# Performance work log

Hardware: AMD Instinct MI355X
Metric: run time of the kernel (lower is better)

The kernel has to match this reference:

```python
import jax, jax.numpy as jnp
import numpy as np

HEADS = 2
OUT_CH = 128
NEG_SLOPE_ATT = 0.2   # GATv2Conv attention LeakyReLU
NEG_SLOPE_ACT = 0.01  # nn.LeakyReLU default
BN_EPS = 1e-5


def setup_inputs() -> dict:
    key = jax.random.key(0)
    ks = jax.random.split(key, 8)
    B, C, D, H, W = 2, 128, 8, 32, 32
    N = B * D * H * W            # 16384 graph nodes
    E = 196608                   # avg degree 12
    x = jax.random.normal(ks[0], (B, C, D, H, W), dtype=jnp.float32)
    edge_index = jax.random.randint(ks[1], (2, E), 0, N, dtype=jnp.int64)
    lin_w = jax.random.normal(ks[2], (C, HEADS * OUT_CH), dtype=jnp.float32) * (1.0 / np.sqrt(C))
    lin_b = jax.random.normal(ks[3], (HEADS * OUT_CH,), dtype=jnp.float32) * 0.02
    att = jax.random.normal(ks[4], (HEADS, OUT_CH), dtype=jnp.float32) * (1.0 / np.sqrt(OUT_CH))
    gat_bias = jax.random.normal(ks[5], (OUT_CH,), dtype=jnp.float32) * 0.02
    bn_gamma = jnp.ones((OUT_CH,), dtype=jnp.float32)
    bn_beta = jnp.zeros((OUT_CH,), dtype=jnp.float32)
    return {"x": x, "edge_index": edge_index, "lin_w": lin_w, "lin_b": lin_b,
            "att": att, "gat_bias": gat_bias, "bn_gamma": bn_gamma, "bn_beta": bn_beta}


def _gatv2(xf, src, dst, lin_w, lin_b, att, gat_bias, n_nodes):
    # shared-weights GATv2: x' = x W + b, per edge e=(j->i): score = a . lrelu(x'_i + x'_j)
    h = (xf @ lin_w + lin_b).reshape(n_nodes, HEADS, OUT_CH)  # [N, H, C]
    x_src = h[src]                                            # [E, H, C] messages
    logits = jnp.einsum('ehc,hc->eh', jax.nn.leaky_relu(x_src + h[dst], NEG_SLOPE_ATT), att)
    # segment softmax over edges sharing the same target node
    m = jax.ops.segment_max(logits, dst, num_segments=n_nodes)      # [N, H]
    ex = jnp.exp(logits - m[dst])
    denom = jax.ops.segment_sum(ex, dst, num_segments=n_nodes)      # [N, H]
    alpha = ex / denom[dst]
    out = jax.ops.segment_sum(x_src * alpha[..., None], dst, num_segments=n_nodes)  # [N, H, C]
    return out.mean(axis=1) + gat_bias  # concat=False -> head mean


def reference(x, edge_index, lin_w, lin_b, att, gat_bias, bn_gamma, bn_beta):
    B, C, D, H, W = x.shape
    N = B * D * H * W
    xf = x.reshape(B, C, -1).transpose(0, 2, 1).reshape(N, C)
    # add_self_loops=True (PyG default)
    loop = jnp.arange(N, dtype=edge_index.dtype)
    src = jnp.concatenate([edge_index[0], loop])
    dst = jnp.concatenate([edge_index[1], loop])
    out = _gatv2(xf, src, dst, lin_w, lin_b, att, gat_bias, N)      # [N, OUT_CH]
    out = out.reshape(B, D * H * W, OUT_CH).transpose(0, 2, 1).reshape(B, OUT_CH, D, H, W)
    # BatchNorm3d (training-mode batch stats, biased variance)
    mean = out.mean(axis=(0, 2, 3, 4), keepdims=True)
    var = out.var(axis=(0, 2, 3, 4), keepdims=True)
    out = (out - mean) / jnp.sqrt(var + BN_EPS)
    out = out * bn_gamma.reshape(1, -1, 1, 1, 1) + bn_beta.reshape(1, -1, 1, 1, 1)
    return jax.nn.leaky_relu(out, NEG_SLOPE_ACT)
```

## Files before the change

kernel.cpp:

```cpp
#include <hip/hip_runtime.h>
#include <math.h>

#define N_NODES 16384
#define CIN 128
#define HOUT 256
#define OUTC 128
#define NEG_ATT 0.2f
#define NEG_ACT 0.01f
#define BN_EPS 1e-5f

typedef short short8 __attribute__((ext_vector_type(8)));
typedef float f32x4 __attribute__((ext_vector_type(4)));

static __device__ __forceinline__ unsigned short f2bf(float f) {
    unsigned int u = __float_as_uint(f);
    unsigned int r = (u + 0x7FFFu + ((u >> 16) & 1u)) >> 16;
    return (unsigned short)r;
}
static __device__ __forceinline__ float bf2f(unsigned short s) {
    return __uint_as_float(((unsigned int)s) << 16);
}
static __device__ __forceinline__ void loadbf8(const unsigned short* p, float* f) {
    uint4 u = *(const uint4*)p;
    f[0] = __uint_as_float(u.x << 16);
    f[1] = __uint_as_float(u.x & 0xffff0000u);
    f[2] = __uint_as_float(u.y << 16);
    f[3] = __uint_as_float(u.y & 0xffff0000u);
    f[4] = __uint_as_float(u.z << 16);
    f[5] = __uint_as_float(u.z & 0xffff0000u);
    f[6] = __uint_as_float(u.w << 16);
    f[7] = __uint_as_float(u.w & 0xffff0000u);
}

#define LDP 136
__global__ __launch_bounds__(256) void gemm_kernel(const float* __restrict__ x,
                                                   const float* __restrict__ lin_w,
                                                   const float* __restrict__ lin_b,
                                                   unsigned short* __restrict__ h,
                                                   int* __restrict__ deg,
                                                   float* __restrict__ gz) {
    __shared__ __align__(16) unsigned short A_s[64 * LDP];
    __shared__ __align__(16) unsigned short Bt_s[64 * LDP];
    const int t = threadIdx.x;
    const int bid = blockIdx.x;

    if (t < 16) deg[bid * 16 + t] = 0;
    if (bid == 0) gz[t] = 0.f;

    const int node0 = (bid >> 2) * 64;
    const int o0 = (bid & 3) * 64;
    const int b = node0 >> 13;
    const int s0 = node0 & 8191;

    const int nt = t & 15;
    const int kt = t >> 4;
#pragma unroll
    for (int p = 0; p < 2; p++) {
        const int kb = p * 64 + kt * 4;
        float4 ar[4], br[4];
#pragma unroll
        for (int r = 0; r < 4; r++) {
            ar[r] = *(const float4*)&x[((b * CIN + kb + r) << 13) + s0 + nt * 4];
            br[r] = *(const float4*)&lin_w[(kb + r) * HOUT + o0 + nt * 4];
        }
#pragma unroll
        for (int j = 0; j < 4; j++) {
            ushort4 va, vb;
            va.x = f2bf(((const float*)&ar[0])[j]);
            va.y = f2bf(((const float*)&ar[1])[j]);
            va.z = f2bf(((const float*)&ar[2])[j]);
            va.w = f2bf(((const float*)&ar[3])[j]);
            vb.x = f2bf(((const float*)&br[0])[j]);
            vb.y = f2bf(((const float*)&br[1])[j]);
            vb.z = f2bf(((const float*)&br[2])[j]);
            vb.w = f2bf(((const float*)&br[3])[j]);
            *(ushort4*)&A_s[(nt * 4 + j) * LDP + kb] = va;
            *(ushort4*)&Bt_s[(nt * 4 + j) * LDP + kb] = vb;
        }
    }
    __syncthreads();

    const int w = t >> 6;
    const int lane = t & 63;
    const int lrow = lane & 15;
    const int lquad = lane >> 4;
    const int m0 = w * 16;

    short8 afr[4];
#pragma unroll
    for (int ks = 0; ks < 4; ks++)
        afr[ks] = *(const short8*)&A_s[(m0 + lrow) * LDP + ks * 32 + lquad * 8];

    f32x4 acc[4];
#pragma unroll
    for (int c = 0; c < 4; c++) { acc[c][0] = 0.f; acc[c][1] = 0.f; acc[c][2] = 0.f; acc[c][3] = 0.f; }

#pragma unroll
    for (int c = 0; c < 4; c++) {
#pragma unroll
        for (int ks = 0; ks < 4; ks++) {
            short8 bfr = *(const short8*)&Bt_s[(c * 16 + lrow) * LDP + ks * 32 + lquad * 8];
            acc[c] = __builtin_amdgcn_mfma_f32_16x16x32_bf16(afr[ks], bfr, acc[c], 0, 0, 0);
        }
    }

#pragma unroll
    for (int c = 0; c < 4; c++) {
        const int col = o0 + c * 16 + lrow;
        const float lb = lin_b[col];
#pragma unroll
        for (int r = 0; r < 4; r++) {
            const int n = node0 + m0 + lquad * 4 + r;
            h[n * HOUT + col] = f2bf(acc[c][r] + lb);
        }
    }
}

__global__ void count_kernel(const int* __restrict__ dst, int* __restrict__ deg, int E) {
    int e = blockIdx.x * 256 + threadIdx.x;
    if (e < E) atomicAdd(&deg[dst[e]], 1);
}

__global__ __launch_bounds__(1024) void scan_kernel(const int* __restrict__ deg,
                                                    int* __restrict__ row_ptr,
                                                    int* __restrict__ cursor) {
    __shared__ int sums[1024];
    const int t = threadIdx.x;
    int local[16];
    int s = 0;
#pragma unroll
    for (int k = 0; k < 16; k++) {
        local[k] = deg[t * 16 + k];
        s += local[k];
    }
    sums[t] = s;
    __syncthreads();
    for (int off = 1; off < 1024; off <<= 1) {
        int v = (t >= off) ? sums[t - off] : 0;
        __syncthreads();
        sums[t] += v;
        __syncthreads();
    }
    int run = sums[t] - s;
#pragma unroll
    for (int k = 0; k < 16; k++) {
        row_ptr[t * 16 + k] = run;
        cursor[t * 16 + k] = run;
        run += local[k];
    }
    if (t == 1023) row_ptr[N_NODES] = run;
}

__global__ void scatter_kernel(const int* __restrict__ edges, int* __restrict__ cursor,
                               int* __restrict__ csr, int E) {
    int e = blockIdx.x * 256 + threadIdx.x;
    if (e < E) {
        int s = edges[e];
        int d = edges[E + e];
        int p = atomicAdd(&cursor[d], 1);
        csr[p] = s;
    }
}

__global__ __launch_bounds__(256) void gat_kernel(const unsigned short* __restrict__ h,
                                                  const int* __restrict__ row_ptr,
                                                  const int* __restrict__ csr,
                                                  const float* __restrict__ att,
                                                  const float* __restrict__ gat_bias,
                                                  float* __restrict__ gat,
                                                  float* __restrict__ gsum,
                                                  float* __restrict__ gsumsq) {
    const int t = threadIdx.x;
    const int lane = t & 63;
    const int w = t >> 6;
    const int half = lane >> 5;
    const int sub = lane & 31;
    const int c0 = sub * 8;

    __shared__ float ssum[128], ssq[128];
    if (t < 128) { ssum[t] = 0.f; ssq[t] = 0.f; }
    __syncthreads();

    float av[8];
    *(float4*)&av[0] = *(const float4*)&att[c0];
    *(float4*)&av[4] = *(const float4*)&att[c0 + 4];
    float gb[8];
    *(float4*)&gb[0] = *(const float4*)&gat_bias[c0 & 127];
    *(float4*)&gb[4] = *(const float4*)&gat_bias[(c0 & 127) + 4];

    float st[8] = {}, sq[8] = {};

    for (int i = 0; i < 4; i++) {
        const int node = (blockIdx.x << 4) + (w << 2) + i;
        float hd[8];
        loadbf8(&h[node * HOUT + c0], hd);
        const int beg = row_ptr[node];
        const int cntT = row_ptr[node + 1] - beg + 1;
        float denom = 0.f;
        float acc[8] = {};

        for (int base = 0; base < cntT; base += 8) {
            int ei[4];
            int jj[4];
#pragma unroll
            for (int u = 0; u < 4; u++) {
                ei[u] = base + 2 * u + half;
                jj[u] = (ei[u] == 0) ? node : ((ei[u] < cntT) ? csr[beg + ei[u] - 1] : node);
            }
            float hj[4][8];
            float p[4];
#pragma unroll
            for (int u = 0; u < 4; u++) {
                loadbf8(&h[jj[u] * HOUT + c0], hj[u]);
                float d = 0.f;
#pragma unroll
                for (int c = 0; c < 8; c++) {
                    float v = hj[u][c] + hd[c];
                    v = fmaxf(v, NEG_ATT * v);
                    d = fmaf(v, av[c], d);
                }
                p[u] = d;
            }
#pragma unroll
            for (int s = 1; s <= 8; s <<= 1) {
#pragma unroll
                for (int u = 0; u < 4; u++) p[u] += __shfl_xor(p[u], s);
            }
#pragma unroll
            for (int u = 0; u < 4; u++) {
                float wt = (ei[u] < cntT) ? __expf(p[u]) : 0.f;
                denom += wt;
#pragma unroll
                for (int c = 0; c < 8; c++) acc[c] = fmaf(wt, hj[u][c], acc[c]);
            }
        }
        denom += __shfl_xor(denom, 32);
#pragma unroll
        for (int c = 0; c < 8; c++) acc[c] += __shfl_xor(acc[c], 32);
        float inv = 1.0f / denom;
        float r[8];
#pragma unroll
        for (int c = 0; c < 8; c++) r[c] = acc[c] * inv;
#pragma unroll
        for (int c = 0; c < 8; c++) r[c] += __shfl_xor(r[c], 16);
        if (lane < 16) {
            float o[8];
#pragma unroll
            for (int c = 0; c < 8; c++) {
                o[c] = 0.5f * r[c] + gb[c];
                st[c] += o[c];
                sq[c] += o[c] * o[c];
            }
            *(float4*)&gat[node * OUTC + c0] = *(float4*)&o[0];
            *(float4*)&gat[node * OUTC + c0 + 4] = *(float4*)&o[4];
        }
    }
    if (lane < 16) {
#pragma unroll
        for (int c = 0; c < 8; c++) {
            atomicAdd(&ssum[c0 + c], st[c]);
            atomicAdd(&ssq[c0 + c], sq[c]);
        }
    }
    __syncthreads();
    if (t < 128) {
        atomicAdd(&gsum[t], ssum[t]);
        atomicAdd(&gsumsq[t], ssq[t]);
    }
}

__global__ __launch_bounds__(256) void epilogue_kernel(const float* __restrict__ gat,
                                                       const float* __restrict__ gsum,
                                                       const float* __restrict__ gsumsq,
                                                       const float* __restrict__ gamma,
                                                       const float* __restrict__ beta,
                                                       float* __restrict__ out) {
    __shared__ float tile[64 * 129];
    __shared__ float sc[128], sh[128];
    const int t = threadIdx.x;
    if (t < 128) {
        const float invN = 1.0f / (float)N_NODES;
        float mean = gsum[t] * invN;
        float var = gsumsq[t] * invN - mean * mean;
        float rstd = rsqrtf(var + BN_EPS);
        float s = gamma[t] * rstd;
        sc[t] = s;
        sh[t] = beta[t] - mean * s;
    }
    __syncthreads();
    const int n0 = blockIdx.x * 64;
    const int b = n0 >> 13;
    const int s0 = n0 & 8191;
#pragma unroll
    for (int k = 0; k < 32; k++) {
        int f = t + k * 256;
        int nl = f >> 7;
        int c = f & 127;
        float v = gat[(n0 << 7) + f];
        v = v * sc[c] + sh[c];
        v = v > 0.f ? v : NEG_ACT * v;
        tile[nl * 129 + c] = v;
    }
    __syncthreads();
    const int sl = t & 63;
    const int c0 = t >> 6;
#pragma unroll
    for (int k = 0; k < 32; k++) {
        int c = c0 + (k << 2);
        out[((b * OUTC + c) << 13) + s0 + sl] = tile[sl * 129 + c];
    }
}

extern "C" void kernel_launch(void* const* d_in, const int* in_sizes, int n_in,
                              void* d_out, int out_size, void* d_ws, size_t ws_size,
                              hipStream_t stream) {
    const float* x        = (const float*)d_in[0];
    const int*   edges    = (const int*)d_in[1];
    const float* lin_w    = (const float*)d_in[2];
    const float* lin_b    = (const float*)d_in[3];
    const float* att      = (const float*)d_in[4];
    const float* gat_bias = (const float*)d_in[5];
    const float* bn_gamma = (const float*)d_in[6];
    const float* bn_beta  = (const float*)d_in[7];
    float* out = (float*)d_out;
    int E = in_sizes[1] / 2;

    char* ws = (char*)d_ws;
    unsigned short* h = (unsigned short*)(ws);
    float* gat     = (float*)(ws + 8388608);
    int*   deg     = (int*)(ws + 16777216);
    int*   row_ptr = (int*)(ws + 16842752);
    int*   cursor  = (int*)(ws + 16908544);
    int*   csr     = (int*)(ws + 16974080);
    float* gsum    = (float*)(ws + 17825792);
    float* gsumsq  = gsum + 128;

    gemm_kernel<<<1024, 256, 0, stream>>>(x, lin_w, lin_b, h, deg, gsum);
    count_kernel<<<(E + 255) / 256, 256, 0, stream>>>(edges + E, deg, E);
    scan_kernel<<<1, 1024, 0, stream>>>(deg, row_ptr, cursor);
    scatter_kernel<<<(E + 255) / 256, 256, 0, stream>>>(edges, cursor, csr, E);
    gat_kernel<<<N_NODES / 16, 256, 0, stream>>>(h, row_ptr, csr, att, gat_bias, gat, gsum, gsumsq);
    epilogue_kernel<<<N_NODES / 64, 256, 0, stream>>>(gat, gsum, gsumsq, bn_gamma, bn_beta, out);
}
```

Before: 158.3 us.

## Assign one node per wave in GAT kernel, prefetch CSR indices, use wave-shuffle scan

```diff
diff --git a/kernel.cpp b/kernel.cpp
--- a/kernel.cpp
+++ b/kernel.cpp
@@ -16,9 +16,6 @@
     unsigned int u = __float_as_uint(f);
     unsigned int r = (u + 0x7FFFu + ((u >> 16) & 1u)) >> 16;
     return (unsigned short)r;
-}
-static __device__ __forceinline__ float bf2f(unsigned short s) {
-    return __uint_as_float(((unsigned int)s) << 16);
 }
 static __device__ __forceinline__ void loadbf8(const unsigned short* p, float* f) {
     uint4 u = *(const uint4*)p;
@@ -124,8 +121,10 @@
 __global__ __launch_bounds__(1024) void scan_kernel(const int* __restrict__ deg,
                                                     int* __restrict__ row_ptr,
                                                     int* __restrict__ cursor) {
-    __shared__ int sums[1024];
+    __shared__ int wsum[16];
     const int t = threadIdx.x;
+    const int lane = t & 63;
+    const int w = t >> 6;
     int local[16];
     int s = 0;
 #pragma unroll
@@ -133,15 +132,26 @@
         local[k] = deg[t * 16 + k];
         s += local[k];
     }
-    sums[t] = s;
-    __syncthreads();
-    for (int off = 1; off < 1024; off <<= 1) {
-        int v = (t >= off) ? sums[t - off] : 0;
-        __syncthreads();
-        sums[t] += v;
-        __syncthreads();
-    }
-    int run = sums[t] - s;
+    int v = s;
+#pragma unroll
+    for (int off = 1; off < 64; off <<= 1) {
+        int u = __shfl_up(v, off);
+        if (lane >= off) v += u;
+    }
+    if (lane == 63) wsum[w] = v;
+    __syncthreads();
+    if (t < 16) {
+        int x = wsum[t];
+        int a = x;
+#pragma unroll
+        for (int off = 1; off < 16; off <<= 1) {
+            int u = __shfl_up(a, off);
+            if (t >= off) a += u;
+        }
+        wsum[t] = a - x;
+    }
+    __syncthreads();
+    int run = wsum[w] + (v - s);
 #pragma unroll
     for (int k = 0; k < 16; k++) {
         row_ptr[t * 16 + k] = run;
@@ -162,7 +172,7 @@
     }
 }
 
-__global__ __launch_bounds__(256) void gat_kernel(const unsigned short* __restrict__ h,
+__global__ __launch_bounds__(512) void gat_kernel(const unsigned short* __restrict__ h,
                                                   const int* __restrict__ row_ptr,
                                                   const int* __restrict__ csr,
                                                   const float* __restrict__ att,
@@ -170,6 +180,7 @@
                                                   float* __restrict__ gat,
                                                   float* __restrict__ gsum,
                                                   float* __restrict__ gsumsq) {
+    __shared__ float psum[8 * 128], psq[8 * 128];
     const int t = threadIdx.x;
     const int lane = t & 63;
     const int w = t >> 6;
@@ -177,95 +188,96 @@
     const int sub = lane & 31;
     const int c0 = sub * 8;
 
-    __shared__ float ssum[128], ssq[128];
-    if (t < 128) { ssum[t] = 0.f; ssq[t] = 0.f; }
-    __syncthreads();
-
     float av[8];
     *(float4*)&av[0] = *(const float4*)&att[c0];
     *(float4*)&av[4] = *(const float4*)&att[c0 + 4];
-    float gb[8];
-    *(float4*)&gb[0] = *(const float4*)&gat_bias[c0 & 127];
-    *(float4*)&gb[4] = *(const float4*)&gat_bias[(c0 & 127) + 4];
-
-    float st[8] = {}, sq[8] = {};
-
-    for (int i = 0; i < 4; i++) {
-        const int node = (blockIdx.x << 4) + (w << 2) + i;
-        float hd[8];
-        loadbf8(&h[node * HOUT + c0], hd);
-        const int beg = row_ptr[node];
-        const int cntT = row_ptr[node + 1] - beg + 1;
-        float denom = 0.f;
-        float acc[8] = {};
-
-        for (int base = 0; base < cntT; base += 8) {
-            int ei[4];
-            int jj[4];
-#pragma unroll
-            for (int u = 0; u < 4; u++) {
-                ei[u] = base + 2 * u + half;
-                jj[u] = (ei[u] == 0) ? node : ((ei[u] < cntT) ? csr[beg + ei[u] - 1] : node);
+
+    const int node = (blockIdx.x << 3) + w;
+    float hd[8];
+    loadbf8(&h[node * HOUT + c0], hd);
+    const int beg = row_ptr[node];
+    const int cnt = row_ptr[node + 1] - beg + 1;
+
+    int pre = node;
+    if (lane > 0 && lane < cnt) pre = csr[beg + lane - 1];
+
+    float denom = 0.f;
+    float acc[8] = {};
+
+    for (int base = 0; base < cnt; base += 8) {
+        int ei[4], jj[4];
+#pragma unroll
+        for (int u = 0; u < 4; u++) {
+            ei[u] = base + 2 * u + half;
+            int s = __shfl(pre, ei[u] & 63);
+            if (ei[u] >= 64 && ei[u] < cnt) s = csr[beg + ei[u] - 1];
+            jj[u] = (ei[u] < cnt) ? s : node;
+        }
+        float hj[4][8];
+#pragma unroll
+        for (int u = 0; u < 4; u++)
+            loadbf8(&h[jj[u] * HOUT + c0], hj[u]);
+        float p[4];
+#pragma unroll
+        for (int u = 0; u < 4; u++) {
+            float d = 0.f;
+#pragma unroll
+            for (int c = 0; c < 8; c++) {
+                float v = hj[u][c] + hd[c];
+                v = fmaxf(v, NEG_ATT * v);
+                d = fmaf(v, av[c], d);
             }
-            float hj[4][8];
-            float p[4];
-#pragma unroll
-            for (int u = 0; u < 4; u++) {
-                loadbf8(&h[jj[u] * HOUT + c0], hj[u]);
-                float d = 0.f;
-#pragma unroll
-                for (int c = 0; c < 8; c++) {
-                    float v = hj[u][c] + hd[c];
-                    v = fmaxf(v, NEG_ATT * v);
-                    d = fmaf(v, av[c], d);
-                }
-                p[u] = d;
-            }
-#pragma unroll
-            for (int s = 1; s <= 8; s <<= 1) {
-#pragma unroll
-                for (int u = 0; u < 4; u++) p[u] += __shfl_xor(p[u], s);
-            }
-#pragma unroll
-            for (int u = 0; u < 4; u++) {
-                float wt = (ei[u] < cntT) ? __expf(p[u]) : 0.f;
-                denom += wt;
-#pragma unroll
-                for (int c = 0; c < 8; c++) acc[c] = fmaf(wt, hj[u][c], acc[c]);
-            }
-        }
-        denom += __shfl_xor(denom, 32);
-#pragma unroll
-        for (int c = 0; c < 8; c++) acc[c] += __shfl_xor(acc[c], 32);
-        float inv = 1.0f / denom;
-        float r[8];
-#pragma unroll
-        for (int c = 0; c < 8; c++) r[c] = acc[c] * inv;
-#pragma unroll
-        for (int c = 0; c < 8; c++) r[c] += __shfl_xor(r[c], 16);
-        if (lane < 16) {
-            float o[8];
-#pragma unroll
-            for (int c = 0; c < 8; c++) {
-                o[c] = 0.5f * r[c] + gb[c];
-                st[c] += o[c];
-                sq[c] += o[c] * o[c];
-            }
-            *(float4*)&gat[node * OUTC + c0] = *(float4*)&o[0];
-            *(float4*)&gat[node * OUTC + c0 + 4] = *(float4*)&o[4];
-        }
-    }
+            p[u] = d;
+        }
+#pragma unroll
+        for (int s = 1; s <= 8; s <<= 1) {
+#pragma unroll
+            for (int u = 0; u < 4; u++) p[u] += __shfl_xor(p[u], s);
+        }
+#pragma unroll
+        for (int u = 0; u < 4; u++) {
+            float wt = (ei[u] < cnt) ? __expf(p[u]) : 0.f;
+            denom += wt;
+#pragma unroll
+            for (int c = 0; c < 8; c++) acc[c] = fmaf(wt, hj[u][c], acc[c]);
+        }
+    }
+    denom += __shfl_xor(denom, 32);
+#pragma unroll
+    for (int c = 0; c < 8; c++) acc[c] += __shfl_xor(acc[c], 32);
+    float inv = 1.0f / denom;
+    float r[8];
+#pragma unroll
+    for (int c = 0; c < 8; c++) r[c] = acc[c] * inv;
+#pragma unroll
+    for (int c = 0; c < 8; c++) r[c] += __shfl_xor(r[c], 16);
     if (lane < 16) {
+        float gb[8];
+        *(float4*)&gb[0] = *(const float4*)&gat_bias[c0];
+        *(float4*)&gb[4] = *(const float4*)&gat_bias[c0 + 4];
+        float o[8], q[8];
 #pragma unroll
         for (int c = 0; c < 8; c++) {
-            atomicAdd(&ssum[c0 + c], st[c]);
-            atomicAdd(&ssq[c0 + c], sq[c]);
-        }
+            o[c] = 0.5f * r[c] + gb[c];
+            q[c] = o[c] * o[c];
+        }
+        *(float4*)&gat[node * OUTC + c0] = *(float4*)&o[0];
+        *(float4*)&gat[node * OUTC + c0 + 4] = *(float4*)&o[4];
+        *(float4*)&psum[w * 128 + c0] = *(float4*)&o[0];
+        *(float4*)&psum[w * 128 + c0 + 4] = *(float4*)&o[4];
+        *(float4*)&psq[w * 128 + c0] = *(float4*)&q[0];
+        *(float4*)&psq[w * 128 + c0 + 4] = *(float4*)&q[4];
     }
     __syncthreads();
     if (t < 128) {
-        atomicAdd(&gsum[t], ssum[t]);
-        atomicAdd(&gsumsq[t], ssq[t]);
+        float s = 0.f, q = 0.f;
+#pragma unroll
+        for (int k = 0; k < 8; k++) {
+            s += psum[k * 128 + t];
+            q += psq[k * 128 + t];
+        }
+        atomicAdd(&gsum[t], s);
+        atomicAdd(&gsumsq[t], q);
     }
 }
 
@@ -339,6 +351,6 @@
     count_kernel<<<(E + 255) / 256, 256, 0, stream>>>(edges + E, deg, E);
     scan_kernel<<<1, 1024, 0, stream>>>(deg, row_ptr, cursor);
     scatter_kernel<<<(E + 255) / 256, 256, 0, stream>>>(edges, cursor, csr, E);
-    gat_kernel<<<N_NODES / 16, 256, 0, stream>>>(h, row_ptr, csr, att, gat_bias, gat, gsum, gsumsq);
+    gat_kernel<<<N_NODES / 8, 512, 0, stream>>>(h, row_ptr, csr, att, gat_bias, gat, gsum, gsumsq);
     epilogue_kernel<<<N_NODES / 64, 256, 0, stream>>>(gat, gsum, gsumsq, bn_gamma, bn_beta, out);
 }
```

After: 171.9 us. 1.09x slower.
